# Performance work log

Hardware: AMD Instinct MI355X
Metric: run time of the kernel (lower is better)

Reference implementation:

```python
import jax, jax.numpy as jnp
import numpy as np

EMBED_DIM = 64
NUM_HEADS = 8
D_K = EMBED_DIM // NUM_HEADS  # n_wires = 8, state dim 2**8 = 256


def _rx_gate(theta):
    # theta: scalar or [N]; returns [..., 2, 2] complex64
    c = jnp.cos(theta / 2).astype(jnp.complex64)
    s = (-1j) * jnp.sin(theta / 2).astype(jnp.complex64)
    return jnp.stack([jnp.stack([c, s], -1), jnp.stack([s, c], -1)], -2)


def _rz_gate(theta):
    e0 = jnp.exp(-1j * theta.astype(jnp.complex64) / 2)
    e1 = jnp.exp(1j * theta.astype(jnp.complex64) / 2)
    z = jnp.zeros_like(e0)
    return jnp.stack([jnp.stack([e0, z], -1), jnp.stack([z, e1], -1)], -2)


def _apply_1q(state, gate, wire):
    # state: [N] + [2]*n ; gate [2,2] (shared) or [N,2,2] (per-token)
    s = jnp.moveaxis(state, 1 + wire, 1)
    if gate.ndim == 2:
        s = jnp.einsum('ab,nb...->na...', gate, s)
    else:
        s = jnp.einsum('nab,nb...->na...', gate, s)
    return jnp.moveaxis(s, 1, 1 + wire)


def _apply_cnot(state, ctrl, tgt):
    s0 = jax.lax.index_in_dim(state, 0, axis=1 + ctrl, keepdims=True)
    s1 = jax.lax.index_in_dim(state, 1, axis=1 + ctrl, keepdims=True)
    s1 = jnp.flip(s1, axis=1 + tgt)
    return jnp.concatenate([s0, s1], axis=1 + ctrl)


def _pauli_z_signs(n):
    idx = np.arange(2 ** n)
    bits = (idx[None, :] >> (n - 1 - np.arange(n)[:, None])) & 1  # [n, 2**n]
    return jnp.asarray(1.0 - 2.0 * bits, dtype=jnp.float32)


def _qlayer(tokens, params_rx, params_rz):
    # tokens: [N, n] float32 -> PauliZ expectations [N, n]
    N, n = tokens.shape
    depth = params_rx.shape[0]
    state = jnp.zeros((N,) + (2,) * n, dtype=jnp.complex64)
    state = state.at[(slice(None),) + (0,) * n].set(1.0)
    # data-encoding RX per wire (per-token angle)
    for w in range(n):
        state = _apply_1q(state, _rx_gate(tokens[:, w]), w)
    for l in range(depth):
        for w in range(n):
            state = _apply_1q(state, _rx_gate(params_rx[l, w]), w)
            state = _apply_1q(state, _rz_gate(params_rz[l, w]), w)
        for w in range(n - 1):
            state = _apply_cnot(state, w, w + 1)
        state = _apply_cnot(state, n - 1, 0)
    probs = jnp.abs(state.reshape(N, -1)) ** 2  # [N, 2**n]
    signs = _pauli_z_signs(n)  # [n, 2**n]
    return probs @ signs.T  # [N, n]


def setup_inputs() -> dict:
    key = jax.random.key(0)
    k1, k2, k3, k4 = jax.random.split(key, 4)
    B, S = 4, 512
    depth = 2
    return {
        'x': jax.random.normal(k1, (B, S, EMBED_DIM), dtype=jnp.float32),
        'params_rx': jax.random.normal(k2, (depth, D_K), dtype=jnp.float32),
        'params_rz': jax.random.normal(k3, (depth, D_K), dtype=jnp.float32),
        'W_combine': jax.random.normal(k4, (EMBED_DIM, EMBED_DIM), dtype=jnp.float32) * 0.05,
    }


def reference(x, params_rx, params_rz, W_combine):
    B, S, E = x.shape
    H, dk = NUM_HEADS, D_K
    # separate_heads: [B,S,E] -> [B,H,S,dk], then flatten all tokens
    xh = x.reshape(B, S, H, dk).transpose(0, 2, 1, 3)
    tokens = xh.reshape(B * H * S, dk)
    out = _qlayer(tokens, params_rx, params_rz)  # [N, dk]
    out = out.reshape(B, H, S, dk).transpose(0, 2, 1, 3).reshape(B, S, E)
    return out @ W_combine.T
```

## Files before the change

kernel.cpp:

```cpp
#include <hip/hip_runtime.h>


struct C2 { float re, im; };
__device__ __forceinline__ C2 cmul(C2 a, C2 b){ return {a.re*b.re - a.im*b.im, a.re*b.im + a.im*b.re}; }
__device__ __forceinline__ C2 cadd(C2 a, C2 b){ return {a.re+b.re, a.im+b.im}; }
__device__ __forceinline__ C2 csc (C2 a, float k){ return {a.re*k, a.im*k}; }

__host__ __device__ constexpr int phmul(int a, int b) {
    if (a == 0 || b == 0 || a == b) return 0;
    if ((a == 1 && b == 2) || (a == 2 && b == 3) || (a == 3 && b == 1)) return 1;
    return 3;
}

template<int A, int B, int Cc, int D>
__device__ __forceinline__ C2 pexp(const float* m) {
    constexpr int p1 = phmul(A, B);          constexpr int c1 = A ^ B;
    constexpr int p2 = p1 + phmul(c1, Cc);   constexpr int c2 = c1 ^ Cc;
    constexpr int p3 = p2 + phmul(c2, D);    constexpr int c3 = c2 ^ D;
    constexpr int ph = p3 & 3;
    float v = m[c3];
    C2 r{0.f, 0.f};
    if constexpr (ph == 0) r.re = v;
    else if constexpr (ph == 1) r.im = v;
    else if constexpr (ph == 2) r.re = -v;
    else r.im = -v;
    return r;
}

struct V2 { C2 gz, gy; };

template<int LEAD, int TZ>
__device__ __forceinline__ void mstep(V2& v, const float* mr, float kcr, float ksr) {
    C2 hz = cadd(cmul(v.gz, pexp<LEAD,0,3,TZ>(mr)), cmul(v.gy, pexp<LEAD,1,3,TZ>(mr)));
    C2 hy = cadd(cmul(v.gz, pexp<LEAD,0,2,TZ>(mr)), cmul(v.gy, pexp<LEAD,1,2,TZ>(mr)));
    v.gz = csc(hz, kcr); v.gy = csc(hy, ksr);
}

__device__ __forceinline__ float closeO(const V2& v, const float* mn, float szv) {
    return (v.gz.re * mn[3] - v.gy.im * mn[2]) * szv;
}

template<int Bz, int By, int Cc, int D>
__device__ __forceinline__ void w1step(V2& v, const float* m1, float kc1, float ks1) {
    C2 hz = cadd(cmul(v.gz, pexp<3,Bz,Cc,D>(m1)), cmul(v.gy, pexp<2,Bz,Cc,D>(m1)));
    C2 hy = cadd(cmul(v.gz, pexp<3,By,Cc,D>(m1)), cmul(v.gy, pexp<2,By,Cc,D>(m1)));
    v.gz = csc(hz, kc1); v.gy = csc(hy, ks1);
}

__global__ __launch_bounds__(64)
void MultiHeadAttentionQuantum_65481071396433_kernel(
        const float* __restrict__ x,
        const float* __restrict__ prx,
        const float* __restrict__ prz,
        const float* __restrict__ W,
        float* __restrict__ out,
        int depth)
{
    __shared__ float cf[40];
    __shared__ float qs[8][64];
    const int tid = threadIdx.x;

    if (tid < 8) {
        int w = tid;
        float sp, cp;
        __sincosf(prz[w], &sp, &cp);
        cf[w] = cp; cf[8 + w] = sp;
        cf[16 + w] = prx[w];
        float s1, c1;
        __sincosf(prx[(depth - 1) * 8 + w], &s1, &c1);
        cf[24 + w] = c1; cf[32 + w] = s1;
    }
    __syncthreads();

    const int t = blockIdx.x * 64 + tid;
    const float4* xp = (const float4*)(x + t * 8);
    float4 xa = xp[0], xb = xp[1];
    float th[8] = {xa.x, xa.y, xa.z, xa.w, xb.x, xb.y, xb.z, xb.w};

    float m[8][4];
    float kc[8], ks[8];
#pragma unroll
    for (int w = 0; w < 8; ++w) {
        float st, ct;
        __sincosf(th[w] + cf[16 + w], &st, &ct);
        m[w][0] = 1.f;
        m[w][1] = st * cf[8 + w];
        m[w][2] = -st * cf[w];
        m[w][3] = ct;
        kc[w] = cf[24 + w]; ks[w] = cf[32 + w];
    }
    float SZ[9];
    SZ[8] = 1.f;
#pragma unroll
    for (int r = 7; r >= 3; --r) SZ[r] = SZ[r + 1] * m[r][3];

    float q[8];

    {
        V2 F;
        F.gz = csc(pexp<0,3,0,0>(m[0]), kc[0]);
        F.gy = csc(pexp<1,3,0,0>(m[0]), ks[0]);
        w1step<3,2,0,0>(F, m[1], kc[1], ks[1]);
        V2 R;
        R.gz = csc(pexp<0,2,0,0>(m[0]), kc[0]);
        R.gy = csc(pexp<1,2,0,0>(m[0]), ks[0]);
        w1step<3,2,3,2>(R, m[1], kc[1], ks[1]);

        q[1] = closeO(F, m[2], SZ[3]);
        mstep<3,3>(F, m[2], kc[2], ks[2]);  mstep<3,3>(R, m[2], kc[2], ks[2]);
        mstep<3,0>(F, m[3], kc[3], ks[3]);  mstep<3,0>(R, m[3], kc[3], ks[3]);
        q[3] = closeO(F, m[4], SZ[5]);
        mstep<3,3>(F, m[4], kc[4], ks[4]);  mstep<3,3>(R, m[4], kc[4], ks[4]);
        mstep<3,0>(F, m[5], kc[5], ks[5]);  mstep<3,0>(R, m[5], kc[5], ks[5]);
        q[5] = closeO(F, m[6], SZ[7]);
        mstep<3,3>(F, m[6], kc[6], ks[6]);  mstep<3,3>(R, m[6], kc[6], ks[6]);
        float tz = F.gz.re - F.gy.re * m[7][1];
        float ty = R.gz.im * m[7][1] - R.gy.im;
        q[7] = tz * kc[7] - ty * ks[7];
    }

    {
        V2 E;
        E.gz = csc(pexp<0,0,0,0>(m[0]), kc[0]);
        E.gy = csc(pexp<1,0,0,0>(m[0]), ks[0]);
        w1step<3,2,3,0>(E, m[1], kc[1], ks[1]);
        mstep<3,0>(E, m[2], kc[2], ks[2]);
        q[2] = closeO(E, m[3], SZ[4]);
        mstep<3,3>(E, m[3], kc[3], ks[3]);
        mstep<3,0>(E, m[4], kc[4], ks[4]);
        q[4] = closeO(E, m[5], SZ[6]);
        mstep<3,3>(E, m[5], kc[5], ks[5]);
        mstep<3,0>(E, m[6], kc[6], ks[6]);
        q[6] = closeO(E, m[7], SZ[8]);
    }

    {
        V2 Zc, Yc;
        Zc.gz = csc(pexp<3,0,0,0>(m[1]), kc[1] * m[0][3]);
        Zc.gy = csc(pexp<2,0,0,0>(m[1]), ks[1] * m[0][3]);
        Yc.gz = csc(pexp<3,3,2,0>(m[1]), kc[1] * m[0][2]);
        Yc.gy = csc(pexp<2,3,2,0>(m[1]), ks[1] * m[0][2]);
        mstep<0,3>(Zc, m[2], kc[2], ks[2]);  mstep<0,3>(Yc, m[2], kc[2], ks[2]);
        mstep<0,0>(Zc, m[3], kc[3], ks[3]);  mstep<0,0>(Yc, m[3], kc[3], ks[3]);
        mstep<0,3>(Zc, m[4], kc[4], ks[4]);  mstep<0,3>(Yc, m[4], kc[4], ks[4]);
        mstep<0,0>(Zc, m[5], kc[5], ks[5]);  mstep<0,0>(Yc, m[5], kc[5], ks[5]);
        mstep<0,3>(Zc, m[6], kc[6], ks[6]);  mstep<0,3>(Yc, m[6], kc[6], ks[6]);
        float tz = Zc.gz.re * m[7][3] + Zc.gy.im * m[7][2];
        float ty = Yc.gz.re * m[7][2] - Yc.gy.im * m[7][3];
        q[0] = tz * kc[7] - ty * ks[7];
    }

    const int rl = tid >> 3, h = tid & 7;
#pragma unroll
    for (int w = 0; w < 8; ++w) qs[rl][h * 8 + w] = q[w];
    __syncthreads();

    const int e = tid;
    const float4* Wr = (const float4*)(W + e * 64);
    float4 wreg[16];
#pragma unroll
    for (int j = 0; j < 16; ++j) wreg[j] = Wr[j];
    const int row0 = blockIdx.x * 8;
#pragma unroll
    for (int r = 0; r < 8; ++r) {
        const float4* qr = (const float4*)qs[r];
        float acc = 0.f;
#pragma unroll
        for (int j = 0; j < 16; ++j) {
            float4 qv = qr[j];
            float4 wv = wreg[j];
            acc = fmaf(qv.x, wv.x, acc);
            acc = fmaf(qv.y, wv.y, acc);
            acc = fmaf(qv.z, wv.z, acc);
            acc = fmaf(qv.w, wv.w, acc);
        }
        out[(row0 + r) * 64 + e] = acc;
    }
}

extern "C" void kernel_launch(void* const* d_in, const int* in_sizes, int n_in,
                              void* d_out, int out_size, void* d_ws, size_t ws_size,
                              hipStream_t stream) {
    const float* x   = (const float*)d_in[0];
    const float* prx = (const float*)d_in[1];
    const float* prz = (const float*)d_in[2];
    const float* W   = (const float*)d_in[3];
    float* out = (float*)d_out;

    int depth  = in_sizes[1] / 8;
    int tokens = in_sizes[0] / 8;
    int blocks = tokens / 64;

    MultiHeadAttentionQuantum_65481071396433_kernel<<<blocks, 64, 0, stream>>>(
        x, prx, prz, W, out, depth);
}
```

Before: 62.69 us.

## Split per-token circuit evaluation across four wavefronts per block

```diff
diff --git a/kernel.cpp b/kernel.cpp
--- a/kernel.cpp
+++ b/kernel.cpp
@@ -47,7 +47,7 @@
     v.gz = csc(hz, kc1); v.gy = csc(hy, ks1);
 }
 
-__global__ __launch_bounds__(64)
+__global__ __launch_bounds__(256)
 void MultiHeadAttentionQuantum_65481071396433_kernel(
         const float* __restrict__ x,
         const float* __restrict__ prx,
@@ -58,7 +58,17 @@
 {
     __shared__ float cf[40];
     __shared__ float qs[8][64];
+    __shared__ float t7y[64];
+
     const int tid = threadIdx.x;
+    const int fam = tid >> 6;
+    const int lt  = tid & 63;
+
+    const int e = lt;
+    const float4* Wr = (const float4*)(W + e * 64);
+    float4 wreg[16];
+#pragma unroll
+    for (int j = 0; j < 16; ++j) wreg[j] = Wr[j];
 
     if (tid < 8) {
         int w = tid;
@@ -72,7 +82,7 @@
     }
     __syncthreads();
 
-    const int t = blockIdx.x * 64 + tid;
+    const int t = blockIdx.x * 64 + lt;
     const float4* xp = (const float4*)(x + t * 8);
     float4 xa = xp[0], xb = xp[1];
     float th[8] = {xa.x, xa.y, xa.z, xa.w, xb.x, xb.y, xb.z, xb.w};
@@ -94,47 +104,50 @@
 #pragma unroll
     for (int r = 7; r >= 3; --r) SZ[r] = SZ[r + 1] * m[r][3];
 
-    float q[8];
-
-    {
+    const int rl = lt >> 3, hh = lt & 7;
+    float* qrow = &qs[rl][hh * 8];
+
+    if (fam == 0) {
         V2 F;
         F.gz = csc(pexp<0,3,0,0>(m[0]), kc[0]);
         F.gy = csc(pexp<1,3,0,0>(m[0]), ks[0]);
         w1step<3,2,0,0>(F, m[1], kc[1], ks[1]);
+        qrow[1] = closeO(F, m[2], SZ[3]);
+        mstep<3,3>(F, m[2], kc[2], ks[2]);
+        mstep<3,0>(F, m[3], kc[3], ks[3]);
+        qrow[3] = closeO(F, m[4], SZ[5]);
+        mstep<3,3>(F, m[4], kc[4], ks[4]);
+        mstep<3,0>(F, m[5], kc[5], ks[5]);
+        qrow[5] = closeO(F, m[6], SZ[7]);
+        mstep<3,3>(F, m[6], kc[6], ks[6]);
+        float tz = F.gz.re - F.gy.re * m[7][1];
+        qrow[7] = tz * kc[7];
+    } else if (fam == 1) {
         V2 R;
         R.gz = csc(pexp<0,2,0,0>(m[0]), kc[0]);
         R.gy = csc(pexp<1,2,0,0>(m[0]), ks[0]);
         w1step<3,2,3,2>(R, m[1], kc[1], ks[1]);
-
-        q[1] = closeO(F, m[2], SZ[3]);
-        mstep<3,3>(F, m[2], kc[2], ks[2]);  mstep<3,3>(R, m[2], kc[2], ks[2]);
-        mstep<3,0>(F, m[3], kc[3], ks[3]);  mstep<3,0>(R, m[3], kc[3], ks[3]);
-        q[3] = closeO(F, m[4], SZ[5]);
-        mstep<3,3>(F, m[4], kc[4], ks[4]);  mstep<3,3>(R, m[4], kc[4], ks[4]);
-        mstep<3,0>(F, m[5], kc[5], ks[5]);  mstep<3,0>(R, m[5], kc[5], ks[5]);
-        q[5] = closeO(F, m[6], SZ[7]);
-        mstep<3,3>(F, m[6], kc[6], ks[6]);  mstep<3,3>(R, m[6], kc[6], ks[6]);
-        float tz = F.gz.re - F.gy.re * m[7][1];
+        mstep<3,3>(R, m[2], kc[2], ks[2]);
+        mstep<3,0>(R, m[3], kc[3], ks[3]);
+        mstep<3,3>(R, m[4], kc[4], ks[4]);
+        mstep<3,0>(R, m[5], kc[5], ks[5]);
+        mstep<3,3>(R, m[6], kc[6], ks[6]);
         float ty = R.gz.im * m[7][1] - R.gy.im;
-        q[7] = tz * kc[7] - ty * ks[7];
-    }
-
-    {
+        t7y[lt] = ty * ks[7];
+    } else if (fam == 2) {
         V2 E;
         E.gz = csc(pexp<0,0,0,0>(m[0]), kc[0]);
         E.gy = csc(pexp<1,0,0,0>(m[0]), ks[0]);
         w1step<3,2,3,0>(E, m[1], kc[1], ks[1]);
         mstep<3,0>(E, m[2], kc[2], ks[2]);
-        q[2] = closeO(E, m[3], SZ[4]);
+        qrow[2] = closeO(E, m[3], SZ[4]);
         mstep<3,3>(E, m[3], kc[3], ks[3]);
         mstep<3,0>(E, m[4], kc[4], ks[4]);
-        q[4] = closeO(E, m[5], SZ[6]);
+        qrow[4] = closeO(E, m[5], SZ[6]);
         mstep<3,3>(E, m[5], kc[5], ks[5]);
         mstep<3,0>(E, m[6], kc[6], ks[6]);
-        q[6] = closeO(E, m[7], SZ[8]);
-    }
-
-    {
+        qrow[6] = closeO(E, m[7], SZ[8]);
+    } else {
         V2 Zc, Yc;
         Zc.gz = csc(pexp<3,0,0,0>(m[1]), kc[1] * m[0][3]);
         Zc.gy = csc(pexp<2,0,0,0>(m[1]), ks[1] * m[0][3]);
@@ -147,22 +160,19 @@
         mstep<0,3>(Zc, m[6], kc[6], ks[6]);  mstep<0,3>(Yc, m[6], kc[6], ks[6]);
         float tz = Zc.gz.re * m[7][3] + Zc.gy.im * m[7][2];
         float ty = Yc.gz.re * m[7][2] - Yc.gy.im * m[7][3];
-        q[0] = tz * kc[7] - ty * ks[7];
-    }
-
-    const int rl = tid >> 3, h = tid & 7;
-#pragma unroll
-    for (int w = 0; w < 8; ++w) qs[rl][h * 8 + w] = q[w];
+        qrow[0] = tz * kc[7] - ty * ks[7];
+    }
     __syncthreads();
 
-    const int e = tid;
-    const float4* Wr = (const float4*)(W + e * 64);
-    float4 wreg[16];
-#pragma unroll
-    for (int j = 0; j < 16; ++j) wreg[j] = Wr[j];
+    if (tid < 64) {
+        qs[tid >> 3][(tid & 7) * 8 + 7] -= t7y[tid];
+    }
+    __syncthreads();
+
     const int row0 = blockIdx.x * 8;
 #pragma unroll
-    for (int r = 0; r < 8; ++r) {
+    for (int rr = 0; rr < 2; ++rr) {
+        const int r = fam + rr * 4;
         const float4* qr = (const float4*)qs[r];
         float acc = 0.f;
 #pragma unroll
@@ -191,6 +201,6 @@
     int tokens = in_sizes[0] / 8;
     int blocks = tokens / 64;
 
-    MultiHeadAttentionQuantum_65481071396433_kernel<<<blocks, 64, 0, stream>>>(
+    MultiHeadAttentionQuantum_65481071396433_kernel<<<blocks, 256, 0, stream>>>(
         x, prx, prz, W, out, depth);
 }
```

After: 61.53 us. No clear change (-1.8%).
